# Performance work log

Measured on AMD Instinct MI355X. Metric: run time of the kernel, lower is better.

Reference implementation:

```python
import jax, jax.numpy as jnp
import numpy as np

NUM_NODES = 50000
NUM_EDGES = 800000
HIDDEN = 128
HEADS = 8
HEAD_DIM = HIDDEN // HEADS  # 16
FF_HIDDEN = 4 * HIDDEN
LN_EPS = 1e-5


def _xavier(key, shape, gain=0.01):
    fan_out, fan_in = shape
    bound = gain * np.sqrt(6.0 / (fan_in + fan_out))
    return jax.random.uniform(key, shape, jnp.float32, -bound, bound)


def setup_inputs() -> dict:
    key = jax.random.key(0)
    ks = jax.random.split(key, 10)
    x = jax.random.normal(ks[0], (NUM_NODES, HIDDEN), jnp.float32)
    edge_index = jax.random.randint(ks[1], (2, NUM_EDGES), 0, NUM_NODES, jnp.int64)
    return {
        "x": x,
        "edge_index": edge_index,
        "Wq": _xavier(ks[2], (HIDDEN, HIDDEN)),
        "bq": jnp.zeros((HIDDEN,), jnp.float32),
        "Wk": _xavier(ks[3], (HIDDEN, HIDDEN)),
        "bk": jnp.zeros((HIDDEN,), jnp.float32),
        "Wv": _xavier(ks[4], (HIDDEN, HIDDEN)),
        "bv": jnp.zeros((HIDDEN,), jnp.float32),
        "Wo": _xavier(ks[5], (HIDDEN, HIDDEN)),
        "bo": jnp.zeros((HIDDEN,), jnp.float32),
        "W1": _xavier(ks[6], (FF_HIDDEN, HIDDEN)),
        "b1": jnp.zeros((FF_HIDDEN,), jnp.float32),
        "W2": _xavier(ks[7], (HIDDEN, FF_HIDDEN)),
        "b2": jnp.zeros((HIDDEN,), jnp.float32),
        "g1": jnp.ones((HIDDEN,), jnp.float32),
        "be1": jnp.zeros((HIDDEN,), jnp.float32),
        "g2": jnp.ones((HIDDEN,), jnp.float32),
        "be2": jnp.zeros((HIDDEN,), jnp.float32),
    }


def _layernorm(v, g, b):
    mu = jnp.mean(v, axis=-1, keepdims=True)
    var = jnp.mean(jnp.square(v - mu), axis=-1, keepdims=True)
    return (v - mu) * jax.lax.rsqrt(var + LN_EPS) * g + b


def _forward(x, edge_index, Wq, bq, Wk, bk, Wv, bv, Wo, bo, W1, b1, W2, b2, g1, be1, g2, be2):
    src = edge_index[0]  # key/value side (_j)
    dst = edge_index[1]  # query side (_i), aggregation index
    scale = 1.0 / np.sqrt(HEAD_DIM)

    # Euclidean manifold: GeometricLinear == plain linear
    q = (x @ Wq.T + bq).reshape(NUM_NODES, HEADS, HEAD_DIM)
    k = (x @ Wk.T + bk).reshape(NUM_NODES, HEADS, HEAD_DIM)
    v = (x @ Wv.T + bv).reshape(NUM_NODES, HEADS, HEAD_DIM)

    # per-edge attention scores [E, H]
    alpha = jnp.einsum('ehd,ehd->eh', q[dst], k[src]) * scale
    # segment softmax over destination nodes
    m = jax.ops.segment_max(alpha, dst, num_segments=NUM_NODES)  # [N, H]
    ea = jnp.exp(alpha - m[dst])
    denom = jax.ops.segment_sum(ea, dst, num_segments=NUM_NODES)  # [N, H]
    alpha = ea / (denom[dst] + 1e-16)

    # scatter-add weighted values -> [N, H, D]
    agg = jax.ops.segment_sum(v[src] * alpha[..., None], dst, num_segments=NUM_NODES)
    att = agg.reshape(NUM_NODES, HIDDEN) @ Wo.T + bo

    # residual + norm1 (Euclidean)
    h = _layernorm(x + att, g1, be1)

    # feed-forward: fc1 -> exact GELU -> fc2
    ff = (jax.nn.gelu(h @ W1.T + b1, approximate=False)) @ W2.T + b2

    # residual + norm2
    return _layernorm(h + ff, g2, be2)


def reference(x, edge_index, Wq, bq, Wk, bk, Wv, bv, Wo, bo, W1, b1, W2, b2, g1, be1, g2, be2):
    return _forward(x, edge_index, Wq, bq, Wk, bk, Wv, bv, Wo, bo, W1, b1, W2, b2, g1, be1, g2, be2)
```

## Files before the change

kernel.cpp:

```cpp
#include <hip/hip_runtime.h>
#include <math.h>

#define N_HEADS 8
#define HEAD_DIM 16
#define HID 128
#define QKV_ROWB 512

typedef unsigned short ushort_t;
typedef __attribute__((ext_vector_type(8))) short short8;
typedef __attribute__((ext_vector_type(4))) float floatx4;
typedef __attribute__((ext_vector_type(2))) float f32x2;

#define KV_SCALE 64.0f
#define KV_INV_SCALE 0.015625f

#define W2_SCALE 65536.0f
#define A1_SCALE 512.0f
#define FF2_DESCALE (1.0f / 33554432.0f)

__device__ __forceinline__ ushort_t f2bf(float f) {
    unsigned u = __float_as_uint(f);
    unsigned r = (u + 0x7FFFu + ((u >> 16) & 1u)) >> 16;
    return (ushort_t)r;
}
__device__ __forceinline__ float bf2f(ushort_t u) {
    return __uint_as_float(((unsigned)u) << 16);
}

__device__ __forceinline__ void gld_lds16(const void* g, void* l) {
    __builtin_amdgcn_global_load_lds(
        (const __attribute__((address_space(1))) void*)g,
        (__attribute__((address_space(3))) void*)l, 16, 0, 0);
}

__device__ __forceinline__ float gelu_f(float x) {
    float z = fabsf(x) * 0.70710678118654752f;
    float t = 1.0f / (1.0f + 0.3275911f * z);
    float y = t * (0.254829592f + t * (-0.284496736f + t * (1.421413741f
            + t * (-1.453152027f + t * 1.061405429f))));
    float e = 1.0f - y * __expf(-z * z);
    e = copysignf(e, x);
    return 0.5f * x * (1.0f + e);
}

__global__ __launch_bounds__(256)
void prep_kernel(const float* __restrict__ x,
                 const float* __restrict__ Wq, const float* __restrict__ Wk,
                 const float* __restrict__ Wv, const float* __restrict__ Wo,
                 const float* __restrict__ W1, const float* __restrict__ W2,
                 const float* __restrict__ bq, const float* __restrict__ bk,
                 const float* __restrict__ bv,
                 ushort_t* __restrict__ xfrag, ushort_t* __restrict__ woB,
                 ushort_t* __restrict__ wqkvf,
                 ushort_t* __restrict__ w1frag,
                 unsigned char* __restrict__ w2frag8,
                 float* __restrict__ bqkv, int xchunks)
{
    int i = blockIdx.x * 256 + threadIdx.x;
    if (i < xchunks) {
        int t16 = i >> 8;
        int rem = i & 255;
        int lane = rem & 63;
        int row = t16 * 16 + (lane & 15);
        int k   = (rem >> 6) * 32 + (lane >> 4) * 8;
        const float* s = x + (size_t)row * HID + k;
        short8 v;
#pragma unroll
        for (int e = 0; e < 8; ++e) v[e] = (short)f2bf(s[e]);
        *(short8*)(xfrag + (size_t)i * 8) = v;
        return;
    }
    int j = i - xchunks;
    if (j < 8192) {
        float2 v = ((const float2*)Wo)[j];
        woB[j * 2]     = f2bf(v.x);
        woB[j * 2 + 1] = f2bf(v.y);
        return;
    }
    int b = j - 8192;
    if (b < 6144) {
        int w = b >> 11;
        int rem = b & 2047;
        int t16 = rem >> 8;
        int rem2 = rem & 255;
        int lane = rem2 & 63;
        int row = t16 * 16 + (lane & 15);
        int k   = ((rem2 >> 6) & 3) * 32 + (lane >> 4) * 8;
        const float* W = (w == 0) ? Wq : (w == 1) ? Wk : Wv;
        const float* s = W + (size_t)row * HID + k;
        short8 v;
#pragma unroll
        for (int e = 0; e < 8; ++e) v[e] = (short)f2bf(s[e]);
        *(short8*)(wqkvf + (size_t)b * 8) = v;
        return;
    }
    int c = b - 6144;
    if (c < 8192) {
        int lane = c & 63, tk = c >> 6;
        int t16 = tk >> 2, kst = tk & 3;
        int row = t16 * 16 + (lane & 15);
        int kb  = kst * 32 + (lane >> 4) * 8;
        const float* s = W1 + (size_t)row * HID + kb;
        short8 v;
#pragma unroll
        for (int e = 0; e < 8; ++e) v[e] = (short)f2bf(s[e]);
        *(short8*)(w1frag + (size_t)c * 8) = v;
        return;
    }
    int c2 = c - 8192;
    if (c2 < 8192) {
        int lane = c2 & 63, tk = c2 >> 6;
        int t16 = tk >> 4, kst = tk & 15;
        int row = t16 * 16 + (lane & 15);
        int kb  = kst * 32 + (lane >> 4) * 8;
        const float* s = W2 + (size_t)row * 512 + kb;
        unsigned u0 = 0, u1 = 0;
        u0 = __builtin_amdgcn_cvt_pk_fp8_f32(s[0]*W2_SCALE, s[1]*W2_SCALE, u0, false);
        u0 = __builtin_amdgcn_cvt_pk_fp8_f32(s[2]*W2_SCALE, s[3]*W2_SCALE, u0, true);
        u1 = __builtin_amdgcn_cvt_pk_fp8_f32(s[4]*W2_SCALE, s[5]*W2_SCALE, u1, false);
        u1 = __builtin_amdgcn_cvt_pk_fp8_f32(s[6]*W2_SCALE, s[7]*W2_SCALE, u1, true);
        uint2 o; o.x = u0; o.y = u1;
        *(uint2*)(w2frag8 + (size_t)c2 * 8) = o;
        return;
    }
    int d = c2 - 8192;
    if (d < 384) {
        bqkv[d] = (d < 128) ? bq[d] : (d < 256) ? bk[d - 128] : bv[d - 256];
    }
}

__global__ __launch_bounds__(256)
void count_kernel(const int* __restrict__ dst, int* __restrict__ cnt, int E, int N)
{
    int coh = blockIdx.x & 7;
    int bc  = blockIdx.x >> 3;
    int rr  = (N + 7) >> 3;
    int nlo = coh * rr;
    int nhi = nlo + rr; if (nhi > N) nhi = N;
    int stride = (gridDim.x >> 3) * 256;
    for (int e = bc * 256 + threadIdx.x; e < E; e += stride) {
        int d = dst[e];
        if (d >= nlo && d < nhi) atomicAdd(&cnt[d], 1);
    }
}

__global__ __launch_bounds__(256)
void qkvw_kernel(const ushort_t* __restrict__ xfrag,
                 const ushort_t* __restrict__ wqkvf,
                 const float* __restrict__ bqkv,
                 ushort_t* __restrict__ qkvb, int nt16)
{
    __shared__ __align__(16) ushort_t sT[4][16 * 136];
    const int wave = threadIdx.x >> 6, lane = threadIdx.x & 63;
    const int y = blockIdx.y;
    const int l15 = lane & 15, l4 = lane >> 4;
    const int gt0 = blockIdx.x * 8 + wave * 2;
    const int gt0c = (gt0 < nt16) ? gt0 : nt16 - 1;
    const int gt1c = (gt0 + 1 < nt16) ? gt0 + 1 : nt16 - 1;

    floatx4 acc[2][8];
#pragma unroll
    for (int i = 0; i < 2; ++i)
#pragma unroll
        for (int j = 0; j < 8; ++j) acc[i][j] = (floatx4)(0.f);

    const ushort_t* wf = wqkvf + (size_t)y * 16384;
#pragma unroll
    for (int kst = 0; kst < 4; ++kst) {
        short8 a0 = *(const short8*)&xfrag[(((size_t)gt0c * 4 + kst) * 64 + lane) * 8];
        short8 a1 = *(const short8*)&xfrag[(((size_t)gt1c * 4 + kst) * 64 + lane) * 8];
        short8 bv[8];
#pragma unroll
        for (int j = 0; j < 8; ++j)
            bv[j] = *(const short8*)&wf[(((size_t)j * 4 + kst) * 64 + lane) * 8];
#pragma unroll
        for (int j = 0; j < 8; ++j) {
            acc[0][j] = __builtin_amdgcn_mfma_f32_16x16x32_bf16(a0, bv[j], acc[0][j], 0, 0, 0);
            acc[1][j] = __builtin_amdgcn_mfma_f32_16x16x32_bf16(a1, bv[j], acc[1][j], 0, 0, 0);
        }
    }

    float bb[8];
#pragma unroll
    for (int j = 0; j < 8; ++j) bb[j] = bqkv[y * 128 + j * 16 + l15];

#pragma unroll
    for (int i = 0; i < 2; ++i) {
        const int gt = gt0 + i;
#pragma unroll
        for (int j = 0; j < 8; ++j)
#pragma unroll
            for (int r = 0; r < 4; ++r) {
                float v = acc[i][j][r] + bb[j];
                if (y) v *= KV_SCALE;
                sT[wave][(l4 * 4 + r) * 136 + j * 16 + l15] = f2bf(v);
            }
        if (gt < nt16) {
            if (y == 0) {
#pragma unroll
                for (int c = 0; c < 4; ++c) {
                    int ch = l4 * 4 + c;
                    *(short8*)&qkvb[(size_t)(gt * 16 + l15) * 256 + ch * 8] =
                        *(const short8*)&sT[wave][l15 * 136 + ch * 8];
                }
            } else {
                const int koff = (y - 1) * 8;
#pragma unroll
                for (int c = 0; c < 4; ++c) {
                    int ch = l4 * 4 + c;
                    short8 s = *(const short8*)&sT[wave][l15 * 136 + ch * 8];
                    unsigned u0 = 0, u1 = 0;
                    u0 = __builtin_amdgcn_cvt_pk_fp8_f32(
                             bf2f((ushort_t)s[0]), bf2f((ushort_t)s[1]), u0, false);
                    u0 = __builtin_amdgcn_cvt_pk_fp8_f32(
                             bf2f((ushort_t)s[2]), bf2f((ushort_t)s[3]), u0, true);
                    u1 = __builtin_amdgcn_cvt_pk_fp8_f32(
                             bf2f((ushort_t)s[4]), bf2f((ushort_t)s[5]), u1, false);
                    u1 = __builtin_amdgcn_cvt_pk_fp8_f32(
                             bf2f((ushort_t)s[6]), bf2f((ushort_t)s[7]), u1, true);
                    uint2 o; o.x = u0; o.y = u1;
                    *(uint2*)((char*)qkvb + (size_t)(gt * 16 + l15) * QKV_ROWB
                              + 256 + ch * 16 + koff) = o;
                }
            }
        }
    }
}

template<int MT, int ACT, int LN, int OUTF>
__global__ __launch_bounds__(256)
void gemm_t(const ushort_t* __restrict__ A, int lda, int M,
            const ushort_t* __restrict__ W, int K,
            const float* __restrict__ bias,
            ushort_t* __restrict__ hfragp, ushort_t* __restrict__ outb, int ostride,
            const float* __restrict__ resf, const ushort_t* __restrict__ resb,
            const float* __restrict__ g, const float* __restrict__ be)
{
    constexpr int MI   = MT / 32;
    constexpr int HALF = MT * 64 + 128 * 64;
    constexpr int BNC  = MT * 136;
    constexpr int SB   = (2 * HALF > BNC) ? 2 * HALF : BNC;
    __shared__ __align__(16) ushort_t sbuf[SB];
    __shared__ float pS[LN ? MT : 1][2];
    __shared__ float pQ[LN ? MT : 1][2];

    const int tid  = threadIdx.x;
    const int wave = tid >> 6, lane = tid & 63;
    const int gm0 = blockIdx.x * MT;
    const int o0  = blockIdx.y * 128;
    const int mhalf = wave >> 1, ohalf = wave & 1;

    auto stage = [&](int kc, int h) {
        ushort_t* As = sbuf + h * HALF;
        ushort_t* Ws = As + MT * 64;
#pragma unroll
        for (int it = 0; it < 4; ++it) {
            int s   = it * 256 + tid;
            int ln  = s & 63;
            int grp = s >> 6;
            int tile = grp >> 1, kst = grp & 1;
            int row = tile * 16 + (ln & 15);
            int kk  = kst * 32 + (ln >> 4) * 8;
            gld_lds16(&W[(size_t)(o0 + row) * K + kc + kk],
                      &Ws[(it * 256 + wave * 64) * 8]);
        }
#pragma unroll
        for (int it = 0; it < MT / 32; ++it) {
            int s   = it * 256 + tid;
            int ln  = s & 63;
            int grp = s >> 6;
            int tile = grp >> 1, kst = grp & 1;
            int row = tile * 16 + (ln & 15);
            int kk  = kst * 32 + (ln >> 4) * 8;
            int ar = gm0 + row; if (ar >= M) ar = M - 1;
            gld_lds16(&A[(size_t)ar * lda + kc + kk],
                      &As[(it * 256 + wave * 64) * 8]);
        }
    };

    floatx4 acc[MI][4];
#pragma unroll
    for (int i = 0; i < MI; ++i)
#pragma unroll
        for (int j = 0; j < 4; ++j) acc[i][j] = (floatx4)(0.f);

    const int nk = K >> 6;
    stage(0, 0);
    __syncthreads();
    for (int t = 0; t < nk; ++t) {
        if (t + 1 < nk) stage((t + 1) * 64, (t + 1) & 1);
        const ushort_t* As = sbuf + (t & 1) * HALF;
        const ushort_t* Ws = As + MT * 64;
#pragma unroll
        for (int kst = 0; kst < 2; ++kst) {
            short8 af[MI], wf[4];
#pragma unroll
            for (int i = 0; i < MI; ++i) {
                int mt = mhalf * MI + i;
                af[i] = *(const short8*)&As[((mt * 2 + kst) * 64 + lane) * 8];
            }
#pragma unroll
            for (int j = 0; j < 4; ++j) {
                int ot = ohalf * 4 + j;
                wf[j] = *(const short8*)&Ws[((ot * 2 + kst) * 64 + lane) * 8];
            }
#pragma unroll
            for (int i = 0; i < MI; ++i)
#pragma unroll
                for (int j = 0; j < 4; ++j)
                    acc[i][j] = __builtin_amdgcn_mfma_f32_16x16x32_bf16(
                        af[i], wf[j], acc[i][j], 0, 0, 0);
        }
        __syncthreads();
    }

    ushort_t* B16 = sbuf;

    if (LN) {
#pragma unroll
        for (int j = 0; j < 4; ++j) {
            int oc = (ohalf * 4 + j) * 16 + (lane & 15);
            float bj = bias[oc];
#pragma unroll
            for (int i = 0; i < MI; ++i) {
                int rbase = gm0 + (mhalf * MI + i) * 16 + (lane >> 4) * 4;
#pragma unroll
                for (int r = 0; r < 4; ++r) {
                    int rowc = rbase + r; if (rowc >= M) rowc = M - 1;
                    float rv = resb ? bf2f(resb[(size_t)rowc * HID + oc])
                                    : resf[(size_t)rowc * HID + oc];
                    acc[i][j][r] += bj + rv;
                }
            }
        }
#pragma unroll
        for (int i = 0; i < MI; ++i) {
#pragma unroll
            for (int r = 0; r < 4; ++r) {
                float s1 = acc[i][0][r] + acc[i][1][r] + acc[i][2][r] + acc[i][3][r];
                float s2 = acc[i][0][r] * acc[i][0][r] + acc[i][1][r] * acc[i][1][r]
                         + acc[i][2][r] * acc[i][2][r] + acc[i][3][r] * acc[i][3][r];
                s1 += __shfl_xor(s1, 1); s1 += __shfl_xor(s1, 2);
                s1 += __shfl_xor(s1, 4); s1 += __shfl_xor(s1, 8);
                s2 += __shfl_xor(s2, 1); s2 += __shfl_xor(s2, 2);
                s2 += __shfl_xor(s2, 4); s2 += __shfl_xor(s2, 8);
                if ((lane & 15) == 0) {
                    int rl = (mhalf * MI + i) * 16 + (lane >> 4) * 4 + r;
                    pS[rl][ohalf] = s1;
                    pQ[rl][ohalf] = s2;
                }
            }
        }
        __syncthreads();
#pragma unroll
        for (int i = 0; i < MI; ++i) {
#pragma unroll
            for (int r = 0; r < 4; ++r) {
                int rl = (mhalf * MI + i) * 16 + (lane >> 4) * 4 + r;
                float S = pS[rl][0] + pS[rl][1];
                float Q = pQ[rl][0] + pQ[rl][1];
                float mu = S * (1.f / 128.f);
                float var = Q * (1.f / 128.f) - mu * mu;
                float rstd = rsqrtf(var + 1e-5f);
#pragma unroll
                for (int j = 0; j < 4; ++j) {
                    int oc = (ohalf * 4 + j) * 16 + (lane & 15);
                    acc[i][j][r] = (acc[i][j][r] - mu) * rstd * g[oc] + be[oc];
                }
            }
        }
        __syncthreads();
    }

#pragma unroll
    for (int i = 0; i < MI; ++i)
#pragma unroll
        for (int j = 0; j < 4; ++j) {
            int oc = (ohalf * 4 + j) * 16 + (lane & 15);
            float bj = LN ? 0.f : bias[o0 + oc];
#pragma unroll
            for (int r = 0; r < 4; ++r) {
                int rl = (mhalf * MI + i) * 16 + (lane >> 4) * 4 + r;
                float v = acc[i][j][r] + bj;
                if (ACT) v = gelu_f(v);
                B16[rl * 136 + oc] = f2bf(v);
            }
        }
    __syncthreads();
#pragma unroll
    for (int p = 0; p < MT / 16; ++p) {
        int row = p * 16 + (tid >> 4);
        int ch  = tid & 15;
        if (gm0 + row < M)
            *(short8*)&outb[(size_t)(gm0 + row) * ostride + o0 + ch * 8] =
                *(const short8*)&B16[row * 136 + ch * 8];
    }
    if (LN && hfragp) {
        int kst = tid >> 6, ln = tid & 63;
#pragma unroll
        for (int p = 0; p < MT / 16; ++p) {
            if (gm0 + p * 16 < M) {
                int gt = (gm0 >> 4) + p;
                short8 v = *(const short8*)&B16[(p * 16 + (ln & 15)) * 136
                                                + kst * 32 + (ln >> 4) * 8];
                *(short8*)&hfragp[(((size_t)gt * 4 + kst) * 64 + ln) * 8] = v;
            }
        }
    }
}

__global__ __launch_bounds__(256)
void ff1w_kernel(const ushort_t* __restrict__ hfrag,
                 const ushort_t* __restrict__ w1frag,
                 const float* __restrict__ b1,
                 unsigned char* __restrict__ a1img, int M)
{
    __shared__ __align__(16) ushort_t sT[4][16 * 136];
    const int wave = threadIdx.x >> 6, lane = threadIdx.x & 63;
    const int cg = wave;
    const int nt16 = (M + 15) / 16;
    const int gt0 = blockIdx.x * 2;
    const int gt1 = gt0 + 1;
    const int gt1c = (gt1 < nt16) ? gt1 : nt16 - 1;
    const int l15 = lane & 15, l4 = lane >> 4;

    floatx4 acc[2][8];
#pragma unroll
    for (int i = 0; i < 2; ++i)
#pragma unroll
        for (int j = 0; j < 8; ++j) acc[i][j] = (floatx4)(0.f);

#pragma unroll
    for (int kst = 0; kst < 4; ++kst) {
        short8 a0 = *(const short8*)&hfrag[(((size_t)gt0  * 4 + kst) * 64 + lane) * 8];
        short8 a1 = *(const short8*)&hfrag[(((size_t)gt1c * 4 + kst) * 64 + lane) * 8];
        short8 bv[8];
#pragma unroll
        for (int j = 0; j < 8; ++j)
            bv[j] = *(const short8*)&w1frag[((((size_t)cg * 8 + j) * 4 + kst) * 64 + lane) * 8];
#pragma unroll
        for (int j = 0; j < 8; ++j) {
            acc[0][j] = __builtin_amdgcn_mfma_f32_16x16x32_bf16(a0, bv[j], acc[0][j], 0, 0, 0);
            acc[1][j] = __builtin_amdgcn_mfma_f32_16x16x32_bf16(a1, bv[j], acc[1][j], 0, 0, 0);
        }
    }

    float b1v[8];
#pragma unroll
    for (int j = 0; j < 8; ++j) b1v[j] = b1[cg * 128 + j * 16 + l15];

#pragma unroll
    for (int i = 0; i < 2; ++i) {
        const int gt = i ? gt1 : gt0;
#pragma unroll
        for (int j = 0; j < 8; ++j)
#pragma unroll
            for (int r = 0; r < 4; ++r)
                sT[wave][(l4 * 4 + r) * 136 + j * 16 + l15] =
                    f2bf(gelu_f(acc[i][j][r] + b1v[j]));
        if (gt < nt16) {
#pragma unroll
            for (int q = 0; q < 4; ++q) {
                float v[8];
#pragma unroll
                for (int e = 0; e < 8; ++e)
                    v[e] = bf2f(sT[wave][l15 * 136 + q * 32 + l4 * 8 + e]) * A1_SCALE;
                unsigned u0 = 0, u1 = 0;
                u0 = __builtin_amdgcn_cvt_pk_fp8_f32(v[0], v[1], u0, false);
                u0 = __builtin_amdgcn_cvt_pk_fp8_f32(v[2], v[3], u0, true);
                u1 = __builtin_amdgcn_cvt_pk_fp8_f32(v[4], v[5], u1, false);
                u1 = __builtin_amdgcn_cvt_pk_fp8_f32(v[6], v[7], u1, true);
                uint2 o; o.x = u0; o.y = u1;
                *(uint2*)(a1img + (((size_t)gt * 16 + cg * 4 + q) * 64 + lane) * 8) = o;
            }
        }
    }
}

__global__ __launch_bounds__(256)
void ff2w_kernel(const unsigned char* __restrict__ a1img,
                 const unsigned char* __restrict__ w2frag8,
                 const ushort_t* __restrict__ hb,
                 const float* __restrict__ b2,
                 const float* __restrict__ g, const float* __restrict__ be,
                 float* __restrict__ out, int M)
{
    const int wave = threadIdx.x >> 6, lane = threadIdx.x & 63;
    const int t32 = blockIdx.x * 4 + wave;
    const int nt32 = (M + 31) / 32;
    if (t32 >= nt32) return;
    const int nt16 = (M + 15) / 16;
    const int gt0 = t32 * 2;
    const int gt1c = (gt0 + 1 < nt16) ? gt0 + 1 : nt16 - 1;
    const int l15 = lane & 15, l4 = lane >> 4;

    floatx4 acc[2][8];
#pragma unroll
    for (int i = 0; i < 2; ++i)
#pragma unroll
        for (int j = 0; j < 8; ++j) acc[i][j] = (floatx4)(0.f);

#pragma unroll
    for (int kst = 0; kst < 16; ++kst) {
        long a0 = *(const long*)(a1img + (((size_t)gt0  * 16 + kst) * 64 + lane) * 8);
        long a1 = *(const long*)(a1img + (((size_t)gt1c * 16 + kst) * 64 + lane) * 8);
        long bv[8];
#pragma unroll
        for (int j = 0; j < 8; ++j)
            bv[j] = *(const long*)(w2frag8 + (((size_t)j * 16 + kst) * 64 + lane) * 8);
#pragma unroll
        for (int j = 0; j < 8; ++j) {
            acc[0][j] = __builtin_amdgcn_mfma_f32_16x16x32_fp8_fp8(a0, bv[j], acc[0][j], 0, 0, 0);
            acc[1][j] = __builtin_amdgcn_mfma_f32_16x16x32_fp8_fp8(a1, bv[j], acc[1][j], 0, 0, 0);
        }
    }

    float b2v[8], gv[8], bev[8];
#pragma unroll
    for (int j = 0; j < 8; ++j) {
        int oc = j * 16 + l15;
        b2v[j] = b2[oc]; gv[j] = g[oc]; bev[j] = be[oc];
    }

#pragma unroll
    for (int i = 0; i < 2; ++i) {
        const int rb = (t32 * 2 + i) * 16;
#pragma unroll
        for (int j = 0; j < 8; ++j) {
            int oc = j * 16 + l15;
#pragma unroll
            for (int r = 0; r < 4; ++r) {
                int row = rb + l4 * 4 + r;
                int rc = (row < M) ? row : M - 1;
                acc[i][j][r] = acc[i][j][r] * FF2_DESCALE + b2v[j]
                             + bf2f(hb[(size_t)rc * HID + oc]);
            }
        }
#pragma unroll
        for (int r = 0; r < 4; ++r) {
            float s1 = 0.f, s2 = 0.f;
#pragma unroll
            for (int j = 0; j < 8; ++j) {
                s1 += acc[i][j][r];
                s2 += acc[i][j][r] * acc[i][j][r];
            }
            s1 += __shfl_xor(s1, 1); s1 += __shfl_xor(s1, 2);
            s1 += __shfl_xor(s1, 4); s1 += __shfl_xor(s1, 8);
            s2 += __shfl_xor(s2, 1); s2 += __shfl_xor(s2, 2);
            s2 += __shfl_xor(s2, 4); s2 += __shfl_xor(s2, 8);
            float mu = s1 * (1.f / 128.f);
            float var = s2 * (1.f / 128.f) - mu * mu;
            float rstd = rsqrtf(var + 1e-5f);
            int row = rb + l4 * 4 + r;
            if (row < M) {
#pragma unroll
                for (int j = 0; j < 8; ++j)
                    out[(size_t)row * HID + j * 16 + l15] =
                        (acc[i][j][r] - mu) * rstd * gv[j] + bev[j];
            }
        }
    }
}

__global__ __launch_bounds__(256)
void scan1_kernel(const int* __restrict__ cnt, int* __restrict__ parts, int N)
{
    __shared__ int sd[256];
    int t = threadIdx.x;
    int base = blockIdx.x * 1024 + t * 4;
    int s = 0;
#pragma unroll
    for (int j = 0; j < 4; ++j) if (base + j < N) s += cnt[base + j];
    sd[t] = s; __syncthreads();
    for (int off = 128; off; off >>= 1) {
        if (t < off) sd[t] += sd[t + off];
        __syncthreads();
    }
    if (t == 0) parts[blockIdx.x] = sd[0];
}

__global__ __launch_bounds__(256)
void scan2_kernel(const int* __restrict__ parts, int* __restrict__ poff, int nb)
{
    __shared__ int sd[256];
    int t = threadIdx.x;
    int v = (t < nb) ? parts[t] : 0;
    sd[t] = v; __syncthreads();
    for (int off = 1; off < 256; off <<= 1) {
        int u = (t >= off) ? sd[t - off] : 0;
        __syncthreads();
        sd[t] += u;
        __syncthreads();
    }
    if (t < nb) poff[t] = sd[t] - v;
}

__global__ __launch_bounds__(256)
void scan3_kernel(const int* __restrict__ cnt, const int* __restrict__ poff,
                  int* __restrict__ rp, int N)
{
    __shared__ int sd[256];
    int t = threadIdx.x;
    int base = blockIdx.x * 1024 + t * 4;
    int v0 = (base + 0 < N) ? cnt[base + 0] : 0;
    int v1 = (base + 1 < N) ? cnt[base + 1] : 0;
    int v2 = (base + 2 < N) ? cnt[base + 2] : 0;
    int v3 = (base + 3 < N) ? cnt[base + 3] : 0;
    int s = v0 + v1 + v2 + v3;
    sd[t] = s; __syncthreads();
    for (int off = 1; off < 256; off <<= 1) {
        int u = (t >= off) ? sd[t - off] : 0;
        __syncthreads();
        sd[t] += u;
        __syncthreads();
    }
    int o = poff[blockIdx.x] + sd[t] - s;
    if (base + 0 < N) rp[base + 0] = o;
    if (base + 1 < N) rp[base + 1] = o + v0;
    if (base + 2 < N) rp[base + 2] = o + v0 + v1;
    if (base + 3 < N) rp[base + 3] = o + v0 + v1 + v2;
}

__global__ __launch_bounds__(256)
void scatter_kernel(const int* __restrict__ src, const int* __restrict__ dst,
                    int* __restrict__ rp, int* __restrict__ ssrc, int E, int N)
{
    int coh = blockIdx.x & 7;
    int bc  = blockIdx.x >> 3;
    int rr  = (N + 7) >> 3;
    int nlo = coh * rr;
    int nhi = nlo + rr; if (nhi > N) nhi = N;
    int stride = (gridDim.x >> 3) * 256;
    for (int e = bc * 256 + threadIdx.x; e < E; e += stride) {
        int d = dst[e];
        if (d >= nlo && d < nhi) {
            int pos = atomicAdd(&rp[d], 1);
            ssrc[pos] = src[e];
        }
    }
}

__global__ __launch_bounds__(256)
void attn_fused_kernel(const ushort_t* __restrict__ qkvb, const int* __restrict__ rp,
                       const int* __restrict__ ssrc, ushort_t* __restrict__ aggb, int N)
{
    int wave = threadIdx.x >> 6, lane = threadIdx.x & 63;
    int n = blockIdx.x * 4 + wave;
    if (n >= N) return;
    int grp = lane >> 4;
    int cb  = (lane & 15) * 16;
    const char* base = (const char*)qkvb;

    short8 qv = *(const short8*)(base + n * QKV_ROWB + cb);
    float q[8];
#pragma unroll
    for (int j = 0; j < 8; ++j) q[j] = bf2f((ushort_t)qv[j]) * (0.25f / KV_SCALE);

    int r0 = n ? rp[n - 1] : 0;
    int r1 = rp[n];
    float acc[8] = {0.f, 0.f, 0.f, 0.f, 0.f, 0.f, 0.f, 0.f};
    float l = 0.f;

    int r = r0;
    for (; r + 8 <= r1; r += 8) {
        int s0 = ssrc[r + grp];
        int s1 = ssrc[r + 4 + grp];
        uint4 kv0 = *(const uint4*)(base + s0 * QKV_ROWB + 256 + cb);
        uint4 kv1 = *(const uint4*)(base + s1 * QKV_ROWB + 256 + cb);

        f32x2 a0 = __builtin_amdgcn_cvt_pk_f32_fp8(kv0.x, false);
        f32x2 a1 = __builtin_amdgcn_cvt_pk_f32_fp8(kv0.x, true);
        f32x2 a2 = __builtin_amdgcn_cvt_pk_f32_fp8(kv0.y, false);
        f32x2 a3 = __builtin_amdgcn_cvt_pk_f32_fp8(kv0.y, true);
        f32x2 b0 = __builtin_amdgcn_cvt_pk_f32_fp8(kv1.x, false);
        f32x2 b1 = __builtin_amdgcn_cvt_pk_f32_fp8(kv1.x, true);
        f32x2 b2 = __builtin_amdgcn_cvt_pk_f32_fp8(kv1.y, false);
        f32x2 b3 = __builtin_amdgcn_cvt_pk_f32_fp8(kv1.y, true);

        float p0 = 0.f, p1 = 0.f;
        p0 = fmaf(q[0], a0.x, p0); p0 = fmaf(q[1], a0.y, p0);
        p0 = fmaf(q[2], a1.x, p0); p0 = fmaf(q[3], a1.y, p0);
        p0 = fmaf(q[4], a2.x, p0); p0 = fmaf(q[5], a2.y, p0);
        p0 = fmaf(q[6], a3.x, p0); p0 = fmaf(q[7], a3.y, p0);
        p1 = fmaf(q[0], b0.x, p1); p1 = fmaf(q[1], b0.y, p1);
        p1 = fmaf(q[2], b1.x, p1); p1 = fmaf(q[3], b1.y, p1);
        p1 = fmaf(q[4], b2.x, p1); p1 = fmaf(q[5], b2.y, p1);
        p1 = fmaf(q[6], b3.x, p1); p1 = fmaf(q[7], b3.y, p1);

        p0 += __shfl_xor(p0, 1);
        p1 += __shfl_xor(p1, 1);
        float e0 = __expf(p0), e1 = __expf(p1);
        l += e0 + e1;

        f32x2 v0 = __builtin_amdgcn_cvt_pk_f32_fp8(kv0.z, false);
        f32x2 v1 = __builtin_amdgcn_cvt_pk_f32_fp8(kv0.z, true);
        f32x2 v2 = __builtin_amdgcn_cvt_pk_f32_fp8(kv0.w, false);
        f32x2 v3 = __builtin_amdgcn_cvt_pk_f32_fp8(kv0.w, true);
        f32x2 w0 = __builtin_amdgcn_cvt_pk_f32_fp8(kv1.z, false);
        f32x2 w1 = __builtin_amdgcn_cvt_pk_f32_fp8(kv1.z, true);
        f32x2 w2 = __builtin_amdgcn_cvt_pk_f32_fp8(kv1.w, false);
        f32x2 w3 = __builtin_amdgcn_cvt_pk_f32_fp8(kv1.w, true);

        acc[0] = fmaf(e0, v0.x, acc[0]); acc[1] = fmaf(e0, v0.y, acc[1]);
        acc[2] = fmaf(e0, v1.x, acc[2]); acc[3] = fmaf(e0, v1.y, acc[3]);
        acc[4] = fmaf(e0, v2.x, acc[4]); acc[5] = fmaf(e0, v2.y, acc[5]);
        acc[6] = fmaf(e0, v3.x, acc[6]); acc[7] = fmaf(e0, v3.y, acc[7]);
        acc[0] = fmaf(e1, w0.x, acc[0]); acc[1] = fmaf(e1, w0.y, acc[1]);
        acc[2] = fmaf(e1, w1.x, acc[2]); acc[3] = fmaf(e1, w1.y, acc[3]);
        acc[4] = fmaf(e1, w2.x, acc[4]); acc[5] = fmaf(e1, w2.y, acc[5]);
        acc[6] = fmaf(e1, w3.x, acc[6]); acc[7] = fmaf(e1, w3.y, acc[7]);
    }
    for (; r < r1; r += 4) {
        int e = r + grp;
        int s = ssrc[(e < r1) ? e : r0];
        uint4 kv = *(const uint4*)(base + s * QKV_ROWB + 256 + cb);
        f32x2 a0 = __builtin_amdgcn_cvt_pk_f32_fp8(kv.x, false);
        f32x2 a1 = __builtin_amdgcn_cvt_pk_f32_fp8(kv.x, true);
        f32x2 a2 = __builtin_amdgcn_cvt_pk_f32_fp8(kv.y, false);
        f32x2 a3 = __builtin_amdgcn_cvt_pk_f32_fp8(kv.y, true);
        float p = 0.f;
        p = fmaf(q[0], a0.x, p); p = fmaf(q[1], a0.y, p);
        p = fmaf(q[2], a1.x, p); p = fmaf(q[3], a1.y, p);
        p = fmaf(q[4], a2.x, p); p = fmaf(q[5], a2.y, p);
        p = fmaf(q[6], a3.x, p); p = fmaf(q[7], a3.y, p);
        p += __shfl_xor(p, 1);
        float ea = (e < r1) ? __expf(p) : 0.f;
        l += ea;
        f32x2 v0 = __builtin_amdgcn_cvt_pk_f32_fp8(kv.z, false);
        f32x2 v1 = __builtin_amdgcn_cvt_pk_f32_fp8(kv.z, true);
        f32x2 v2 = __builtin_amdgcn_cvt_pk_f32_fp8(kv.w, false);
        f32x2 v3 = __builtin_amdgcn_cvt_pk_f32_fp8(kv.w, true);
        acc[0] = fmaf(ea, v0.x, acc[0]); acc[1] = fmaf(ea, v0.y, acc[1]);
        acc[2] = fmaf(ea, v1.x, acc[2]); acc[3] = fmaf(ea, v1.y, acc[3]);
        acc[4] = fmaf(ea, v2.x, acc[4]); acc[5] = fmaf(ea, v2.y, acc[5]);
        acc[6] = fmaf(ea, v3.x, acc[6]); acc[7] = fmaf(ea, v3.y, acc[7]);
    }

#pragma unroll
    for (int j = 0; j < 8; ++j) {
        acc[j] += __shfl_xor(acc[j], 16);
        acc[j] += __shfl_xor(acc[j], 32);
    }
    l += __shfl_xor(l, 16);
    l += __shfl_xor(l, 32);
    float inv = KV_INV_SCALE / (l + 1e-16f);
    if (grp == 0) {
        short8 o;
#pragma unroll
        for (int j = 0; j < 8; ++j) o[j] = (short)f2bf(acc[j] * inv);
        *(short8*)((char*)aggb + n * 256 + cb) = o;
    }
}

extern "C" void kernel_launch(void* const* d_in, const int* in_sizes, int n_in,
                              void* d_out, int out_size, void* d_ws, size_t ws_size,
                              hipStream_t stream)
{
    const float* x  = (const float*)d_in[0];
    const int*   ei = (const int*)d_in[1];
    const float* Wq = (const float*)d_in[2];
    const float* bq = (const float*)d_in[3];
    const float* Wk = (const float*)d_in[4];
    const float* bk = (const float*)d_in[5];
    const float* Wv = (const float*)d_in[6];
    const float* bv = (const float*)d_in[7];
    const float* Wo = (const float*)d_in[8];
    const float* bo = (const float*)d_in[9];
    const float* W1 = (const float*)d_in[10];
    const float* b1 = (const float*)d_in[11];
    const float* W2 = (const float*)d_in[12];
    const float* b2 = (const float*)d_in[13];
    const float* g1 = (const float*)d_in[14];
    const float* be1= (const float*)d_in[15];
    const float* g2 = (const float*)d_in[16];
    const float* be2= (const float*)d_in[17];
    float* out = (float*)d_out;

    const int N = in_sizes[0] / HID;
    const int E = in_sizes[1] / 2;
    const int* srcp = ei;
    const int* dstp = ei + E;

    const size_t NH = (size_t)N * HID;
    float* wsf = (float*)d_ws;

    const int nt16 = (N + 15) / 16;
    const int nt32 = (N + 31) / 32;

    ushort_t* xfrag = (ushort_t*)wsf;
    ushort_t* qkvb  = (ushort_t*)(wsf + NH / 2);
    ushort_t* hfrag = (ushort_t*)(wsf + NH + NH / 2);
    ushort_t* aggb  = (ushort_t*)(wsf + 2 * NH);
    ushort_t* hb    = (ushort_t*)wsf;
    unsigned char* a1img = (unsigned char*)(wsf + NH / 2);

    ushort_t* U       = (ushort_t*)(wsf + 2 * NH + NH / 2);
    ushort_t* woB     = U;
    ushort_t* wqkvf   = U + 16384;
    ushort_t* w1frag  = U + 65536;
    unsigned char* w2frag8 = (unsigned char*)(U + 131072);
    float*    bqkv = (float*)(w2frag8 + 65536);
    int*      rp   = (int*)(bqkv + 384);
    int*      cnt  = rp + (N + 1);
    int*      poff = cnt + N;
    int*      parts= poff + 256;
    int*      ssrc = parts + 256;

    hipMemsetAsync(cnt, 0, N * sizeof(int), stream);
    const int xchunks = nt16 * 256;
    const int ptot = xchunks + 8192 + 6144 + 8192 + 8192 + 384;
    prep_kernel<<<(ptot + 255) / 256, 256, 0, stream>>>(
        x, Wq, Wk, Wv, Wo, W1, W2, bq, bk, bv,
        xfrag, woB, wqkvf, w1frag, w2frag8, bqkv, xchunks);

    count_kernel<<<2048, 256, 0, stream>>>(dstp, cnt, E, N);
    const int nb = (N + 1023) / 1024;
    scan1_kernel<<<nb, 256, 0, stream>>>(cnt, parts, N);
    scan2_kernel<<<1, 256, 0, stream>>>(parts, poff, nb);
    scan3_kernel<<<nb, 256, 0, stream>>>(cnt, poff, rp, N);
    scatter_kernel<<<2048, 256, 0, stream>>>(srcp, dstp, rp, ssrc, E, N);

    qkvw_kernel<<<dim3((nt16 + 7) / 8, 3), 256, 0, stream>>>(
        xfrag, wqkvf, bqkv, qkvb, nt16);

    attn_fused_kernel<<<(N + 3) / 4, 256, 0, stream>>>(qkvb, rp, ssrc, aggb, N);

    const int gx64 = (N + 63) / 64;
    gemm_t<64, 0, 1, 0><<<dim3(gx64, 1), 256, 0, stream>>>(
        aggb, HID, N, woB, HID, bo, hfrag, hb, HID,
        x, nullptr, g1, be1);

    ff1w_kernel<<<nt32, 256, 0, stream>>>(hfrag, w1frag, b1, a1img, N);

    ff2w_kernel<<<(nt32 + 3) / 4, 256, 0, stream>>>(
        a1img, w2frag8, hb, b2, g2, be2, out, N);
}
```

Measured before the change: 322.4 us.

## Write attention output in MFMA fragment layout and use per-wave Wo GEMM

The attention kernel now stores its aggregated output directly in the MFMA fragment layout, and Wo is pre-packed into fragments in the prep kernel. The generic LDS-staged GEMM with a cross-wave LayerNorm reduction is replaced by a wave-independent kernel. Each wave computes a 32-row by 128-column tile, does the full-row LayerNorm with shuffles, and writes both hb and hfrag through a small per-wave LDS transpose. This removes the global-to-LDS staging and block-level syncs, at the cost of every wave loading the Wo fragments straight from global/L2 memory and holding more accumulator registers.

```diff
diff --git a/kernel.cpp b/kernel.cpp
--- a/kernel.cpp
+++ b/kernel.cpp
@@ -25,12 +25,6 @@
 }
 __device__ __forceinline__ float bf2f(ushort_t u) {
     return __uint_as_float(((unsigned)u) << 16);
-}
-
-__device__ __forceinline__ void gld_lds16(const void* g, void* l) {
-    __builtin_amdgcn_global_load_lds(
-        (const __attribute__((address_space(1))) void*)g,
-        (__attribute__((address_space(3))) void*)l, 16, 0, 0);
 }
 
 __device__ __forceinline__ float gelu_f(float x) {
@@ -50,7 +44,7 @@
                  const float* __restrict__ W1, const float* __restrict__ W2,
                  const float* __restrict__ bq, const float* __restrict__ bk,
                  const float* __restrict__ bv,
-                 ushort_t* __restrict__ xfrag, ushort_t* __restrict__ woB,
+                 ushort_t* __restrict__ xfrag, ushort_t* __restrict__ wofrag,
                  ushort_t* __restrict__ wqkvf,
                  ushort_t* __restrict__ w1frag,
                  unsigned char* __restrict__ w2frag8,
@@ -71,13 +65,19 @@
         return;
     }
     int j = i - xchunks;
-    if (j < 8192) {
-        float2 v = ((const float2*)Wo)[j];
-        woB[j * 2]     = f2bf(v.x);
-        woB[j * 2 + 1] = f2bf(v.y);
+    if (j < 2048) {
+        int lane = j & 63, tk = j >> 6;
+        int t16 = tk >> 2, kst = tk & 3;
+        int row = t16 * 16 + (lane & 15);
+        int kb  = kst * 32 + (lane >> 4) * 8;
+        const float* s = Wo + (size_t)row * HID + kb;
+        short8 v;
+#pragma unroll
+        for (int e = 0; e < 8; ++e) v[e] = (short)f2bf(s[e]);
+        *(short8*)(wofrag + (size_t)j * 8) = v;
         return;
     }
-    int b = j - 8192;
+    int b = j - 2048;
     if (b < 6144) {
         int w = b >> 11;
         int rem = b & 2047;
@@ -227,184 +227,98 @@
     }
 }
 
-template<int MT, int ACT, int LN, int OUTF>
-__global__ __launch_bounds__(256)
-void gemm_t(const ushort_t* __restrict__ A, int lda, int M,
-            const ushort_t* __restrict__ W, int K,
-            const float* __restrict__ bias,
-            ushort_t* __restrict__ hfragp, ushort_t* __restrict__ outb, int ostride,
-            const float* __restrict__ resf, const ushort_t* __restrict__ resb,
-            const float* __restrict__ g, const float* __restrict__ be)
-{
-    constexpr int MI   = MT / 32;
-    constexpr int HALF = MT * 64 + 128 * 64;
-    constexpr int BNC  = MT * 136;
-    constexpr int SB   = (2 * HALF > BNC) ? 2 * HALF : BNC;
-    __shared__ __align__(16) ushort_t sbuf[SB];
-    __shared__ float pS[LN ? MT : 1][2];
-    __shared__ float pQ[LN ? MT : 1][2];
-
-    const int tid  = threadIdx.x;
-    const int wave = tid >> 6, lane = tid & 63;
-    const int gm0 = blockIdx.x * MT;
-    const int o0  = blockIdx.y * 128;
-    const int mhalf = wave >> 1, ohalf = wave & 1;
-
-    auto stage = [&](int kc, int h) {
-        ushort_t* As = sbuf + h * HALF;
-        ushort_t* Ws = As + MT * 64;
-#pragma unroll
-        for (int it = 0; it < 4; ++it) {
-            int s   = it * 256 + tid;
-            int ln  = s & 63;
-            int grp = s >> 6;
-            int tile = grp >> 1, kst = grp & 1;
-            int row = tile * 16 + (ln & 15);
-            int kk  = kst * 32 + (ln >> 4) * 8;
-            gld_lds16(&W[(size_t)(o0 + row) * K + kc + kk],
-                      &Ws[(it * 256 + wave * 64) * 8]);
-        }
-#pragma unroll
-        for (int it = 0; it < MT / 32; ++it) {
-            int s   = it * 256 + tid;
-            int ln  = s & 63;
-            int grp = s >> 6;
-            int tile = grp >> 1, kst = grp & 1;
-            int row = tile * 16 + (ln & 15);
-            int kk  = kst * 32 + (ln >> 4) * 8;
-            int ar = gm0 + row; if (ar >= M) ar = M - 1;
-            gld_lds16(&A[(size_t)ar * lda + kc + kk],
-                      &As[(it * 256 + wave * 64) * 8]);
-        }
-    };
-
-    floatx4 acc[MI][4];
-#pragma unroll
-    for (int i = 0; i < MI; ++i)
-#pragma unroll
-        for (int j = 0; j < 4; ++j) acc[i][j] = (floatx4)(0.f);
-
-    const int nk = K >> 6;
-    stage(0, 0);
-    __syncthreads();
-    for (int t = 0; t < nk; ++t) {
-        if (t + 1 < nk) stage((t + 1) * 64, (t + 1) & 1);
-        const ushort_t* As = sbuf + (t & 1) * HALF;
-        const ushort_t* Ws = As + MT * 64;
-#pragma unroll
-        for (int kst = 0; kst < 2; ++kst) {
-            short8 af[MI], wf[4];
-#pragma unroll
-            for (int i = 0; i < MI; ++i) {
-                int mt = mhalf * MI + i;
-                af[i] = *(const short8*)&As[((mt * 2 + kst) * 64 + lane) * 8];
-            }
-#pragma unroll
-            for (int j = 0; j < 4; ++j) {
-                int ot = ohalf * 4 + j;
-                wf[j] = *(const short8*)&Ws[((ot * 2 + kst) * 64 + lane) * 8];
-            }
-#pragma unroll
-            for (int i = 0; i < MI; ++i)
-#pragma unroll
-                for (int j = 0; j < 4; ++j)
-                    acc[i][j] = __builtin_amdgcn_mfma_f32_16x16x32_bf16(
-                        af[i], wf[j], acc[i][j], 0, 0, 0);
-        }
-        __syncthreads();
-    }
-
-    ushort_t* B16 = sbuf;
-
-    if (LN) {
-#pragma unroll
-        for (int j = 0; j < 4; ++j) {
-            int oc = (ohalf * 4 + j) * 16 + (lane & 15);
-            float bj = bias[oc];
-#pragma unroll
-            for (int i = 0; i < MI; ++i) {
-                int rbase = gm0 + (mhalf * MI + i) * 16 + (lane >> 4) * 4;
-#pragma unroll
-                for (int r = 0; r < 4; ++r) {
-                    int rowc = rbase + r; if (rowc >= M) rowc = M - 1;
-                    float rv = resb ? bf2f(resb[(size_t)rowc * HID + oc])
-                                    : resf[(size_t)rowc * HID + oc];
-                    acc[i][j][r] += bj + rv;
-                }
-            }
-        }
-#pragma unroll
-        for (int i = 0; i < MI; ++i) {
+__global__ __launch_bounds__(256)
+void wow_kernel(const ushort_t* __restrict__ aggfrag,
+                const ushort_t* __restrict__ wofrag,
+                const float* __restrict__ bo,
+                const float* __restrict__ x,
+                const float* __restrict__ g, const float* __restrict__ be,
+                ushort_t* __restrict__ hb, ushort_t* __restrict__ hfrag, int M)
+{
+    __shared__ __align__(16) ushort_t sT[4][16 * 136];
+    const int wave = threadIdx.x >> 6, lane = threadIdx.x & 63;
+    const int t32 = blockIdx.x * 4 + wave;
+    const int nt32 = (M + 31) / 32;
+    if (t32 >= nt32) return;
+    const int nt16 = (M + 15) / 16;
+    const int gt0 = t32 * 2;
+    const int gt1c = (gt0 + 1 < nt16) ? gt0 + 1 : nt16 - 1;
+    const int l15 = lane & 15, l4 = lane >> 4;
+
+    floatx4 acc[2][8];
+#pragma unroll
+    for (int i = 0; i < 2; ++i)
+#pragma unroll
+        for (int j = 0; j < 8; ++j) acc[i][j] = (floatx4)(0.f);
+
+#pragma unroll
+    for (int kst = 0; kst < 4; ++kst) {
+        short8 a0 = *(const short8*)&aggfrag[(((size_t)gt0  * 4 + kst) * 64 + lane) * 8];
+        short8 a1 = *(const short8*)&aggfrag[(((size_t)gt1c * 4 + kst) * 64 + lane) * 8];
+        short8 bv[8];
+#pragma unroll
+        for (int j = 0; j < 8; ++j)
+            bv[j] = *(const short8*)&wofrag[(((size_t)j * 4 + kst) * 64 + lane) * 8];
+#pragma unroll
+        for (int j = 0; j < 8; ++j) {
+            acc[0][j] = __builtin_amdgcn_mfma_f32_16x16x32_bf16(a0, bv[j], acc[0][j], 0, 0, 0);
+            acc[1][j] = __builtin_amdgcn_mfma_f32_16x16x32_bf16(a1, bv[j], acc[1][j], 0, 0, 0);
+        }
+    }
+
+    float bov[8], gv[8], bev[8];
+#pragma unroll
+    for (int j = 0; j < 8; ++j) {
+        int oc = j * 16 + l15;
+        bov[j] = bo[oc]; gv[j] = g[oc]; bev[j] = be[oc];
+    }
+
+#pragma unroll
+    for (int i = 0; i < 2; ++i) {
+        const int gt = gt0 + i;
+        const int rb = gt * 16;
+#pragma unroll
+        for (int j = 0; j < 8; ++j) {
+            int oc = j * 16 + l15;
 #pragma unroll
             for (int r = 0; r < 4; ++r) {
-                float s1 = acc[i][0][r] + acc[i][1][r] + acc[i][2][r] + acc[i][3][r];
-                float s2 = acc[i][0][r] * acc[i][0][r] + acc[i][1][r] * acc[i][1][r]
-                         + acc[i][2][r] * acc[i][2][r] + acc[i][3][r] * acc[i][3][r];
-                s1 += __shfl_xor(s1, 1); s1 += __shfl_xor(s1, 2);
-                s1 += __shfl_xor(s1, 4); s1 += __shfl_xor(s1, 8);
-                s2 += __shfl_xor(s2, 1); s2 += __shfl_xor(s2, 2);
-                s2 += __shfl_xor(s2, 4); s2 += __shfl_xor(s2, 8);
-                if ((lane & 15) == 0) {
-                    int rl = (mhalf * MI + i) * 16 + (lane >> 4) * 4 + r;
-                    pS[rl][ohalf] = s1;
-                    pQ[rl][ohalf] = s2;
-                }
-            }
-        }
-        __syncthreads();
-#pragma unroll
-        for (int i = 0; i < MI; ++i) {
-#pragma unroll
-            for (int r = 0; r < 4; ++r) {
-                int rl = (mhalf * MI + i) * 16 + (lane >> 4) * 4 + r;
-                float S = pS[rl][0] + pS[rl][1];
-                float Q = pQ[rl][0] + pQ[rl][1];
-                float mu = S * (1.f / 128.f);
-                float var = Q * (1.f / 128.f) - mu * mu;
-                float rstd = rsqrtf(var + 1e-5f);
-#pragma unroll
-                for (int j = 0; j < 4; ++j) {
-                    int oc = (ohalf * 4 + j) * 16 + (lane & 15);
-                    acc[i][j][r] = (acc[i][j][r] - mu) * rstd * g[oc] + be[oc];
-                }
-            }
-        }
-        __syncthreads();
-    }
-
-#pragma unroll
-    for (int i = 0; i < MI; ++i)
-#pragma unroll
-        for (int j = 0; j < 4; ++j) {
-            int oc = (ohalf * 4 + j) * 16 + (lane & 15);
-            float bj = LN ? 0.f : bias[o0 + oc];
-#pragma unroll
-            for (int r = 0; r < 4; ++r) {
-                int rl = (mhalf * MI + i) * 16 + (lane >> 4) * 4 + r;
-                float v = acc[i][j][r] + bj;
-                if (ACT) v = gelu_f(v);
-                B16[rl * 136 + oc] = f2bf(v);
-            }
-        }
-    __syncthreads();
-#pragma unroll
-    for (int p = 0; p < MT / 16; ++p) {
-        int row = p * 16 + (tid >> 4);
-        int ch  = tid & 15;
-        if (gm0 + row < M)
-            *(short8*)&outb[(size_t)(gm0 + row) * ostride + o0 + ch * 8] =
-                *(const short8*)&B16[row * 136 + ch * 8];
-    }
-    if (LN && hfragp) {
-        int kst = tid >> 6, ln = tid & 63;
-#pragma unroll
-        for (int p = 0; p < MT / 16; ++p) {
-            if (gm0 + p * 16 < M) {
-                int gt = (gm0 >> 4) + p;
-                short8 v = *(const short8*)&B16[(p * 16 + (ln & 15)) * 136
-                                                + kst * 32 + (ln >> 4) * 8];
-                *(short8*)&hfragp[(((size_t)gt * 4 + kst) * 64 + ln) * 8] = v;
-            }
+                int row = rb + l4 * 4 + r;
+                int rc = (row < M) ? row : M - 1;
+                acc[i][j][r] += bov[j] + x[(size_t)rc * HID + oc];
+            }
+        }
+#pragma unroll
+        for (int r = 0; r < 4; ++r) {
+            float s1 = 0.f, s2 = 0.f;
+#pragma unroll
+            for (int j = 0; j < 8; ++j) {
+                s1 += acc[i][j][r];
+                s2 += acc[i][j][r] * acc[i][j][r];
+            }
+            s1 += __shfl_xor(s1, 1); s1 += __shfl_xor(s1, 2);
+            s1 += __shfl_xor(s1, 4); s1 += __shfl_xor(s1, 8);
+            s2 += __shfl_xor(s2, 1); s2 += __shfl_xor(s2, 2);
+            s2 += __shfl_xor(s2, 4); s2 += __shfl_xor(s2, 8);
+            float mu = s1 * (1.f / 128.f);
+            float var = s2 * (1.f / 128.f) - mu * mu;
+            float rstd = rsqrtf(var + 1e-5f);
+#pragma unroll
+            for (int j = 0; j < 8; ++j) {
+                float v = (acc[i][j][r] - mu) * rstd * gv[j] + bev[j];
+                sT[wave][(l4 * 4 + r) * 136 + j * 16 + l15] = f2bf(v);
+            }
+        }
+        if (gt < nt16) {
+#pragma unroll
+            for (int c = 0; c < 4; ++c) {
+                int ch = l4 * 4 + c;
+                *(short8*)&hb[(size_t)(gt * 16 + l15) * HID + ch * 8] =
+                    *(const short8*)&sT[wave][l15 * 136 + ch * 8];
+            }
+#pragma unroll
+            for (int q = 0; q < 4; ++q)
+                *(short8*)&hfrag[(((size_t)gt * 4 + q) * 64 + lane) * 8] =
+                    *(const short8*)&sT[wave][l15 * 136 + q * 32 + l4 * 8];
         }
     }
 }
@@ -642,7 +556,7 @@
 
 __global__ __launch_bounds__(256)
 void attn_fused_kernel(const ushort_t* __restrict__ qkvb, const int* __restrict__ rp,
-                       const int* __restrict__ ssrc, ushort_t* __restrict__ aggb, int N)
+                       const int* __restrict__ ssrc, ushort_t* __restrict__ aggfrag, int N)
 {
     int wave = threadIdx.x >> 6, lane = threadIdx.x & 63;
     int n = blockIdx.x * 4 + wave;
@@ -748,7 +662,9 @@
         short8 o;
 #pragma unroll
         for (int j = 0; j < 8; ++j) o[j] = (short)f2bf(acc[j] * inv);
-        *(short8*)((char*)aggb + n * 256 + cb) = o;
+        int t16 = n >> 4, kst = lane >> 2;
+        int lp = (n & 15) + ((lane & 3) << 4);
+        *(short8*)&aggfrag[(((size_t)t16 * 4 + kst) * 64 + lp) * 8] = o;
     }
 }
 
@@ -787,15 +703,15 @@
     const int nt16 = (N + 15) / 16;
     const int nt32 = (N + 31) / 32;
 
-    ushort_t* xfrag = (ushort_t*)wsf;
-    ushort_t* qkvb  = (ushort_t*)(wsf + NH / 2);
-    ushort_t* hfrag = (ushort_t*)(wsf + NH + NH / 2);
-    ushort_t* aggb  = (ushort_t*)(wsf + 2 * NH);
-    ushort_t* hb    = (ushort_t*)wsf;
+    ushort_t* xfrag   = (ushort_t*)wsf;
+    ushort_t* qkvb    = (ushort_t*)(wsf + NH / 2);
+    ushort_t* hfrag   = (ushort_t*)(wsf + NH + NH / 2);
+    ushort_t* aggfrag = (ushort_t*)(wsf + 2 * NH);
+    ushort_t* hb      = (ushort_t*)wsf;
     unsigned char* a1img = (unsigned char*)(wsf + NH / 2);
 
     ushort_t* U       = (ushort_t*)(wsf + 2 * NH + NH / 2);
-    ushort_t* woB     = U;
+    ushort_t* wofrag  = U;
     ushort_t* wqkvf   = U + 16384;
     ushort_t* w1frag  = U + 65536;
     unsigned char* w2frag8 = (unsigned char*)(U + 131072);
@@ -808,10 +724,10 @@
 
     hipMemsetAsync(cnt, 0, N * sizeof(int), stream);
     const int xchunks = nt16 * 256;
-    const int ptot = xchunks + 8192 + 6144 + 8192 + 8192 + 384;
+    const int ptot = xchunks + 2048 + 6144 + 8192 + 8192 + 384;
     prep_kernel<<<(ptot + 255) / 256, 256, 0, stream>>>(
         x, Wq, Wk, Wv, Wo, W1, W2, bq, bk, bv,
-        xfrag, woB, wqkvf, w1frag, w2frag8, bqkv, xchunks);
+        xfrag, wofrag, wqkvf, w1frag, w2frag8, bqkv, xchunks);
 
     count_kernel<<<2048, 256, 0, stream>>>(dstp, cnt, E, N);
     const int nb = (N + 1023) / 1024;
@@ -823,12 +739,10 @@
     qkvw_kernel<<<dim3((nt16 + 7) / 8, 3), 256, 0, stream>>>(
         xfrag, wqkvf, bqkv, qkvb, nt16);
 
-    attn_fused_kernel<<<(N + 3) / 4, 256, 0, stream>>>(qkvb, rp, ssrc, aggb, N);
-
-    const int gx64 = (N + 63) / 64;
-    gemm_t<64, 0, 1, 0><<<dim3(gx64, 1), 256, 0, stream>>>(
-        aggb, HID, N, woB, HID, bo, hfrag, hb, HID,
-        x, nullptr, g1, be1);
+    attn_fused_kernel<<<(N + 3) / 4, 256, 0, stream>>>(qkvb, rp, ssrc, aggfrag, N);
+
+    wow_kernel<<<(nt32 + 3) / 4, 256, 0, stream>>>(
+        aggfrag, wofrag, bo, x, g1, be1, hb, hfrag, N);
 
     ff1w_kernel<<<nt32, 256, 0, stream>>>(hfrag, w1frag, b1, a1img, N);
 
```

Result: no change. 321.1 us (-0.4%).
